# Performance work log

Measured on AMD Instinct MI355X. Metric: run time of the kernel, lower is better.

Reference implementation:

```python
import jax, jax.numpy as jnp
import numpy as np

N_EMBD = 384
N_HEAD = 6
HEAD_SIZE = N_EMBD // N_HEAD
D_FF = 4 * N_EMBD
LN_EPS = 1e-3  # keras LayerNormalization default epsilon


def setup_inputs() -> dict:
    key = jax.random.key(0)
    ks = jax.random.split(key, 12)
    B, T = 4, 2048
    s = 1.0 / np.sqrt(N_EMBD)
    return {
        "x": jax.random.normal(ks[0], (B, T, N_EMBD), dtype=jnp.float32),
        "Wq": jax.random.normal(ks[1], (N_EMBD, N_EMBD), dtype=jnp.float32) * s,
        "Wk": jax.random.normal(ks[2], (N_EMBD, N_EMBD), dtype=jnp.float32) * s,
        "Wv": jax.random.normal(ks[3], (N_EMBD, N_EMBD), dtype=jnp.float32) * s,
        "Wo": jax.random.normal(ks[4], (N_EMBD, N_EMBD), dtype=jnp.float32) * s,
        "bo": jnp.zeros((N_EMBD,), dtype=jnp.float32),
        "W1": jax.random.normal(ks[5], (N_EMBD, D_FF), dtype=jnp.float32) * s,
        "b1": jnp.zeros((D_FF,), dtype=jnp.float32),
        "W2": jax.random.normal(ks[6], (D_FF, N_EMBD), dtype=jnp.float32) * (1.0 / np.sqrt(D_FF)),
        "b2": jnp.zeros((N_EMBD,), dtype=jnp.float32),
        "g1": jnp.ones((N_EMBD,), dtype=jnp.float32),
        "be1": jnp.zeros((N_EMBD,), dtype=jnp.float32),
        "g2": jnp.ones((N_EMBD,), dtype=jnp.float32),
        "be2": jnp.zeros((N_EMBD,), dtype=jnp.float32),
    }


def _layer_norm(x, gamma, beta):
    mu = jnp.mean(x, axis=-1, keepdims=True)
    var = jnp.mean(jnp.square(x - mu), axis=-1, keepdims=True)
    return (x - mu) * jax.lax.rsqrt(var + LN_EPS) * gamma + beta


def _block(x, Wq, Wk, Wv, Wo, bo, W1, b1, W2, b2, g1, be1, g2, be2):
    B, T, C = x.shape
    H, D = N_HEAD, HEAD_SIZE
    q = (x @ Wq).reshape(B, T, H, D).transpose(0, 2, 1, 3)  # [B,H,T,D]
    k = (x @ Wk).reshape(B, T, H, D).transpose(0, 2, 1, 3)
    v = (x @ Wv).reshape(B, T, H, D).transpose(0, 2, 1, 3)
    scores = jnp.einsum("bhqd,bhkd->bhqk", q, k) / jnp.sqrt(jnp.float32(D))
    causal = jnp.tril(jnp.ones((T, T), dtype=bool))
    scores = jnp.where(causal, scores, jnp.float32(-1e9))
    attn = jax.nn.softmax(scores, axis=-1)  # dropout is identity at inference
    out = jnp.einsum("bhqk,bhkd->bhqd", attn, v)
    out = out.transpose(0, 2, 1, 3).reshape(B, T, H * D)
    y = out @ Wo + bo
    x = _layer_norm(x + y, g1, be1)
    y = jax.nn.relu(x @ W1 + b1) @ W2 + b2
    return _layer_norm(x + y, g2, be2)


def reference(x, Wq, Wk, Wv, Wo, bo, W1, b1, W2, b2, g1, be1, g2, be2):
    return _block(x, Wq, Wk, Wv, Wo, bo, W1, b1, W2, b2, g1, be1, g2, be2)
```

## Files before the change

### kernel.cpp

```cpp
#include <hip/hip_runtime.h>

#define C_DIM  384
#define HEADS  6
#define HD     64
#define FF_DIM 1536
#define LN_EPS 1e-3f
#define TSEQ   2048
#define BATCH  4
#define LOG2E  1.4426950408889634f
#define QK_SCALE 0.18033688011112042f

typedef __attribute__((ext_vector_type(4))) float          f32x4;
typedef __attribute__((ext_vector_type(4))) float          float4_t;
typedef __attribute__((ext_vector_type(8))) short          bfrag;
typedef __attribute__((ext_vector_type(4))) unsigned short ushort4_t;
typedef __attribute__((ext_vector_type(8))) unsigned short ushort8_t;

__device__ inline unsigned short f2bf(float f) {
    unsigned int u = __builtin_bit_cast(unsigned int, f);
    u += 0x7fff + ((u >> 16) & 1);
    return (unsigned short)(u >> 16);
}
__device__ inline unsigned short f2bf_t(float f) {
    return (unsigned short)(__builtin_bit_cast(unsigned int, f) >> 16);
}

__device__ inline void gload_lds16(const void* g, void* l) {
    __builtin_amdgcn_global_load_lds(
        (const __attribute__((address_space(1))) unsigned int*)g,
        (__attribute__((address_space(3))) unsigned int*)l,
        16, 0, 0);
}

__global__ __launch_bounds__(256)
void transpose_w4(const float* __restrict__ Wq, const float* __restrict__ Wk,
                  const float* __restrict__ Wv, const float* __restrict__ Wo,
                  unsigned short* __restrict__ Dq, unsigned short* __restrict__ Dk,
                  unsigned short* __restrict__ Dv, unsigned short* __restrict__ Do_)
{
    __shared__ float tile[32][33];
    const int z = blockIdx.z;
    const float* W = z == 0 ? Wq : (z == 1 ? Wk : (z == 2 ? Wv : Wo));
    unsigned short* D = z == 0 ? Dq : (z == 1 ? Dk : (z == 2 ? Dv : Do_));
    const int tx = threadIdx.x, ty = threadIdx.y;
    const int n0 = blockIdx.x * 32, k0 = blockIdx.y * 32;
    #pragma unroll
    for (int i = 0; i < 32; i += 8)
        tile[ty + i][tx] = W[(size_t)(k0 + ty + i) * C_DIM + n0 + tx];
    __syncthreads();
    #pragma unroll
    for (int i = 0; i < 32; i += 8)
        D[(size_t)(n0 + ty + i) * C_DIM + k0 + tx] = f2bf(tile[tx][ty + i]);
}

__global__ __launch_bounds__(256)
void transpose_w(const float* __restrict__ W, unsigned short* __restrict__ Wt, int K, int N)
{
    __shared__ float tile[32][33];
    const int tx = threadIdx.x, ty = threadIdx.y;
    const int n0 = blockIdx.x * 32, k0 = blockIdx.y * 32;
    #pragma unroll
    for (int i = 0; i < 32; i += 8)
        tile[ty + i][tx] = W[(size_t)(k0 + ty + i) * N + n0 + tx];
    __syncthreads();
    #pragma unroll
    for (int i = 0; i < 32; i += 8)
        Wt[(size_t)(n0 + ty + i) * K + k0 + tx] = f2bf(tile[tx][ty + i]);
}

__global__ __launch_bounds__(256)
void cvt_f32_bf16_x4(const float* __restrict__ in, unsigned short* __restrict__ out, int n4)
{
    int i = blockIdx.x * 256 + threadIdx.x;
    if (i >= n4) return;
    float4_t v = ((const float4_t*)in)[i];
    ushort4_t o = { f2bf(v.x), f2bf(v.y), f2bf(v.z), f2bf(v.w) };
    ((ushort4_t*)out)[i] = o;
}

__global__ __launch_bounds__(256)
void vtrans_kernel(const unsigned short* __restrict__ qkv,
                   unsigned short* __restrict__ vt,
                   unsigned short* __restrict__ ktc)
{
    __shared__ unsigned short tile[32][34];
    const int tx = threadIdx.x, ty = threadIdx.y;
    const int bh = blockIdx.z, b = bh / HEADS, h = bh % HEADS;
    const int t0 = blockIdx.x * 32, d0 = blockIdx.y * 32;
    #pragma unroll
    for (int i = 0; i < 32; i += 8) {
        tile[ty + i][tx] = qkv[(size_t)(b * TSEQ + t0 + ty + i) * 1152 + 2 * C_DIM + h * HD + d0 + tx];
        ktc[((size_t)bh * TSEQ + t0 + ty + i) * HD + d0 + tx] =
            qkv[(size_t)(b * TSEQ + t0 + ty + i) * 1152 + C_DIM + h * HD + d0 + tx];
    }
    __syncthreads();
    #pragma unroll
    for (int i = 0; i < 32; i += 8)
        vt[((size_t)bh * HD + d0 + ty + i) * TSEQ + t0 + tx] = tile[tx][ty + i];
}

template<int OBF16, int BIAS, int RELU, int QSCALE>
__global__ __launch_bounds__(256)
void gemm_lds(const unsigned short* __restrict__ A, const unsigned short* __restrict__ Bt,
              const float* __restrict__ bias, void* __restrict__ Cv,
              int M, int N, int K)
{
    __shared__ __align__(16) unsigned short As[16 * 512];
    __shared__ __align__(16) unsigned short Bs[16 * 512];

    const int t = threadIdx.x, lane = t & 63, w = t >> 6;
    const int ln16 = lane & 15, hi16 = lane >> 4;
    const int wr = w >> 1, wc = w & 1;
    const int row0 = blockIdx.y * 128, col0 = blockIdx.x * 128;

    f32x4 acc[4][4] = {};

    for (int k0 = 0; k0 < K; k0 += 64) {
        #pragma unroll
        for (int i = 0; i < 4; ++i) {
            const int f  = w * 4 + i;
            const int ks = f >> 3, rf = f & 7;
            const int row = rf * 16 + ln16;
            const int kc  = k0 + ks * 32 + hi16 * 8;
            gload_lds16(&A [(size_t)(row0 + row) * K + kc], &As[f * 512]);
            gload_lds16(&Bt[(size_t)(col0 + row) * K + kc], &Bs[f * 512]);
        }
        __syncthreads();
        #pragma unroll
        for (int ks = 0; ks < 2; ++ks) {
            bfrag a[4], b[4];
            #pragma unroll
            for (int i = 0; i < 4; ++i)
                a[i] = *(const bfrag*)&As[(ks * 8 + wr * 4 + i) * 512 + lane * 8];
            #pragma unroll
            for (int j = 0; j < 4; ++j)
                b[j] = *(const bfrag*)&Bs[(ks * 8 + wc * 4 + j) * 512 + lane * 8];
            #pragma unroll
            for (int i = 0; i < 4; ++i)
                #pragma unroll
                for (int j = 0; j < 4; ++j)
                    acc[i][j] = __builtin_amdgcn_mfma_f32_16x16x32_bf16(a[i], b[j], acc[i][j], 0, 0, 0);
        }
        __syncthreads();
    }

    #pragma unroll
    for (int j = 0; j < 4; ++j) {
        const int col = col0 + wc * 64 + j * 16 + ln16;
        const float bv = BIAS ? bias[col] : 0.0f;
        const float sc = (QSCALE && col < C_DIM) ? QK_SCALE : 1.0f;
        #pragma unroll
        for (int i = 0; i < 4; ++i) {
            #pragma unroll
            for (int e = 0; e < 4; ++e) {
                const int row = row0 + wr * 64 + i * 16 + hi16 * 4 + e;
                float v = acc[i][j][e] + bv;
                if (RELU) v = fmaxf(v, 0.0f);
                if (QSCALE) v *= sc;
                if (OBF16) ((unsigned short*)Cv)[(size_t)row * N + col] = f2bf(v);
                else       ((float*)Cv)[(size_t)row * N + col] = v;
            }
        }
    }
}

__device__ inline void qk16(const bfrag (&qf)[2][2], const bfrag (&kf)[4][2],
                            f32x4 (&sf)[2][4])
{
    #pragma unroll
    for (int jt = 0; jt < 4; ++jt)
        #pragma unroll
        for (int ks = 0; ks < 2; ++ks) {
            sf[0][jt] = __builtin_amdgcn_mfma_f32_16x16x32_bf16(qf[0][ks], kf[jt][ks], sf[0][jt], 0, 0, 0);
            sf[1][jt] = __builtin_amdgcn_mfma_f32_16x16x32_bf16(qf[1][ks], kf[jt][ks], sf[1][jt], 0, 0, 0);
        }
}

__device__ inline void softmax_pv(f32x4 (&sf)[2][4], const bfrag (&vf)[4][2],
                                  f32x4 (&acc)[2][4],
                                  float (&mrow)[2][4], float (&lrow)[2][4],
                                  unsigned short (*Ps)[72],
                                  int tok0, int kt, bool last, int ln16, int hi16)
{
    float lmax[2][4];
    bool need = false;
    #pragma unroll
    for (int rf = 0; rf < 2; ++rf)
        #pragma unroll
        for (int e = 0; e < 4; ++e) {
            const int row = tok0 + rf * 16 + hi16 * 4 + e;
            float mx = -1e30f;
            #pragma unroll
            for (int jt = 0; jt < 4; ++jt) {
                float sv = sf[rf][jt][e];
                if (last && (kt * 64 + jt * 16 + ln16 > row)) sv = -1e30f;
                mx = fmaxf(mx, sv);
            }
            lmax[rf][e] = mx;
            need = need || (mx > mrow[rf][e] + 8.0f);
        }
    if (__any(need)) {
        #pragma unroll
        for (int rf = 0; rf < 2; ++rf)
            #pragma unroll
            for (int e = 0; e < 4; ++e) {
                float rm = lmax[rf][e];
                rm = fmaxf(rm, __shfl_xor(rm, 1));
                rm = fmaxf(rm, __shfl_xor(rm, 2));
                rm = fmaxf(rm, __shfl_xor(rm, 4));
                rm = fmaxf(rm, __shfl_xor(rm, 8));
                const float mn = fmaxf(mrow[rf][e], rm);
                const float corr = exp2f(mrow[rf][e] - mn);
                mrow[rf][e] = mn;
                lrow[rf][e] *= corr;
                #pragma unroll
                for (int dt = 0; dt < 4; ++dt) acc[rf][dt][e] *= corr;
            }
    }

    #pragma unroll
    for (int rf = 0; rf < 2; ++rf)
        #pragma unroll
        for (int jt = 0; jt < 4; ++jt)
            #pragma unroll
            for (int e = 0; e < 4; ++e) {
                const int row = tok0 + rf * 16 + hi16 * 4 + e;
                float sv = sf[rf][jt][e];
                if (last && (kt * 64 + jt * 16 + ln16 > row)) sv = -1e30f;
                const float pe = exp2f(sv - mrow[rf][e]);
                lrow[rf][e] += pe;
                Ps[rf * 16 + hi16 * 4 + e][jt * 16 + ln16] = f2bf_t(pe);
            }

    bfrag pf[2][2];
    #pragma unroll
    for (int rf = 0; rf < 2; ++rf)
        #pragma unroll
        for (int ks = 0; ks < 2; ++ks)
            pf[rf][ks] = *(const bfrag*)&Ps[rf * 16 + ln16][ks * 32 + hi16 * 8];
    #pragma unroll
    for (int ks = 0; ks < 2; ++ks)
        #pragma unroll
        for (int rf = 0; rf < 2; ++rf)
            #pragma unroll
            for (int dt = 0; dt < 4; ++dt)
                acc[rf][dt] = __builtin_amdgcn_mfma_f32_16x16x32_bf16(pf[rf][ks], vf[dt][ks], acc[rf][dt], 0, 0, 0);
}

__global__ __launch_bounds__(64)
void attn_kernel(const unsigned short* __restrict__ qkv,
                 const unsigned short* __restrict__ ktc,
                 const unsigned short* __restrict__ vt,
                 unsigned short* __restrict__ att)
{
    __shared__ __align__(16) unsigned short Ps[32][72];
    const int lane = threadIdx.x;
    const int ln16 = lane & 15, hi16 = lane >> 4;
    const int bid = blockIdx.x;
    const int xcd = bid & 7;
    const int i2  = bid >> 3;
    const int bh  = xcd * 3 + (i2 >> 6);
    const int qw  = 63 - (i2 & 63);
    const int b   = bh / HEADS, h = bh % HEADS;
    const int tok0 = qw * 32;
    const size_t qrow0 = (size_t)b * TSEQ;
    const int NT = (qw >> 1) + 1;

    bfrag qf[2][2];
    #pragma unroll
    for (int rf = 0; rf < 2; ++rf)
        #pragma unroll
        for (int ks = 0; ks < 2; ++ks)
            qf[rf][ks] = *(const bfrag*)&qkv[(qrow0 + tok0 + rf * 16 + ln16) * 1152 + h * HD + ks * 32 + hi16 * 8];

    f32x4 acc[2][4] = {};
    float mrow[2][4], lrow[2][4];
    #pragma unroll
    for (int rf = 0; rf < 2; ++rf)
        #pragma unroll
        for (int e = 0; e < 4; ++e) { mrow[rf][e] = -1e30f; lrow[rf][e] = 0.0f; }

    const unsigned short* Kb = ktc + (size_t)bh * TSEQ * HD;
    const unsigned short* Vb = vt  + (size_t)bh * HD * TSEQ;

    auto loadK = [&](bfrag (&kf)[4][2], int kt) {
        #pragma unroll
        for (int jt = 0; jt < 4; ++jt)
            #pragma unroll
            for (int ks = 0; ks < 2; ++ks)
                kf[jt][ks] = *(const bfrag*)&Kb[(size_t)(kt * 64 + jt * 16 + ln16) * HD + ks * 32 + hi16 * 8];
    };
    auto loadV = [&](bfrag (&vf)[4][2], int kt) {
        #pragma unroll
        for (int dt = 0; dt < 4; ++dt)
            #pragma unroll
            for (int ks = 0; ks < 2; ++ks)
                vf[dt][ks] = *(const bfrag*)&Vb[(size_t)(dt * 16 + ln16) * TSEQ + kt * 64 + ks * 32 + hi16 * 8];
    };

    bfrag kfa[4][2], vfa[4][2], kfb[4][2], vfb[4][2];
    loadK(kfa, 0); loadV(vfa, 0);
    int kt = 0;
    for (;;) {
        if (kt + 1 < NT) { loadK(kfb, kt + 1); loadV(vfb, kt + 1); }
        {
            f32x4 sf[2][4] = {};
            qk16(qf, kfa, sf);
            softmax_pv(sf, vfa, acc, mrow, lrow, Ps, tok0, kt, kt == NT - 1, ln16, hi16);
        }
        if (++kt >= NT) break;
        if (kt + 1 < NT) { loadK(kfa, kt + 1); loadV(vfa, kt + 1); }
        {
            f32x4 sf[2][4] = {};
            qk16(qf, kfb, sf);
            softmax_pv(sf, vfb, acc, mrow, lrow, Ps, tok0, kt, kt == NT - 1, ln16, hi16);
        }
        if (++kt >= NT) break;
    }

    #pragma unroll
    for (int rf = 0; rf < 2; ++rf)
        #pragma unroll
        for (int e = 0; e < 4; ++e) {
            float l = lrow[rf][e];
            l += __shfl_xor(l, 1);
            l += __shfl_xor(l, 2);
            l += __shfl_xor(l, 4);
            l += __shfl_xor(l, 8);
            const float inv = 1.0f / l;
            const size_t row = qrow0 + tok0 + rf * 16 + hi16 * 4 + e;
            #pragma unroll
            for (int dt = 0; dt < 4; ++dt)
                att[row * C_DIM + h * HD + dt * 16 + ln16] = f2bf(acc[rf][dt][e] * inv);
        }
}

template<int WB>
__global__ __launch_bounds__(256)
void ln_residual_kernel(const float* __restrict__ A, const float* __restrict__ R,
                        const float* __restrict__ gamma, const float* __restrict__ beta,
                        float* __restrict__ out, unsigned short* __restrict__ outb, int Mrows)
{
    const int lane = threadIdx.x & 63;
    const int wv   = threadIdx.x >> 6;
    const int row  = blockIdx.x * 4 + wv;
    if (row >= Mrows) return;
    const size_t off = (size_t)row * C_DIM;

    float v[6];
    float sum = 0.0f;
    #pragma unroll
    for (int j = 0; j < 6; ++j) {
        const int c = lane + 64 * j;
        v[j] = A[off + c] + R[off + c];
        sum += v[j];
    }
    #pragma unroll
    for (int o = 1; o < 64; o <<= 1) sum += __shfl_xor(sum, o);
    const float mu = sum * (1.0f / C_DIM);

    float sq = 0.0f;
    #pragma unroll
    for (int j = 0; j < 6; ++j) { const float d = v[j] - mu; sq = fmaf(d, d, sq); }
    #pragma unroll
    for (int o = 1; o < 64; o <<= 1) sq += __shfl_xor(sq, o);
    const float rstd = rsqrtf(sq * (1.0f / C_DIM) + LN_EPS);

    #pragma unroll
    for (int j = 0; j < 6; ++j) {
        const int c = lane + 64 * j;
        const float r = (v[j] - mu) * rstd * gamma[c] + beta[c];
        out[off + c] = r;
        if (WB) outb[off + c] = f2bf(r);
    }
}

extern "C" void kernel_launch(void* const* d_in, const int* in_sizes, int n_in,
                              void* d_out, int out_size, void* d_ws, size_t ws_size,
                              hipStream_t stream)
{
    const float* x   = (const float*)d_in[0];
    const float* Wq  = (const float*)d_in[1];
    const float* Wk  = (const float*)d_in[2];
    const float* Wv  = (const float*)d_in[3];
    const float* Wo  = (const float*)d_in[4];
    const float* bo  = (const float*)d_in[5];
    const float* W1  = (const float*)d_in[6];
    const float* b1  = (const float*)d_in[7];
    const float* W2  = (const float*)d_in[8];
    const float* b2  = (const float*)d_in[9];
    const float* g1  = (const float*)d_in[10];
    const float* be1 = (const float*)d_in[11];
    const float* g2  = (const float*)d_in[12];
    const float* be2 = (const float*)d_in[13];
    float* out = (float*)d_out;

    const int M = BATCH * TSEQ;
    const size_t MC = (size_t)M * C_DIM;

    char* ws = (char*)d_ws;
    unsigned short* qkv = (unsigned short*)ws;
    unsigned short* vt  = (unsigned short*)(ws + (size_t)M*1152*2);
    unsigned short* att = (unsigned short*)(ws + (size_t)M*1152*2 + (size_t)BATCH*HEADS*HD*TSEQ*2);
    unsigned short* h1  = (unsigned short*)ws;
    char* p2 = ws + (size_t)M*1152*2 + (size_t)BATCH*HEADS*HD*TSEQ*2 + MC*2;
    unsigned short* xb  = (unsigned short*)p2;
    unsigned short* ktc = xb;
    float* y   = (float*)(p2 + MC*2);
    float* x1  = (float*)(p2 + MC*2 + MC*4);
    unsigned short* x1b = (unsigned short*)(p2 + MC*2 + 2*MC*4);
    char* p3 = p2 + MC*2 + 2*MC*4 + MC*2;
    unsigned short* Wqkv_t = (unsigned short*)p3;
    unsigned short* Wo_t   = Wqkv_t + (size_t)3*C_DIM*C_DIM;
    unsigned short* W1_t   = Wo_t   + (size_t)C_DIM*C_DIM;
    unsigned short* W2_t   = W1_t   + (size_t)FF_DIM*C_DIM;

    dim3 b256(256), b328(32, 8);

    transpose_w4<<<dim3(C_DIM/32, C_DIM/32, 4), b328, 0, stream>>>(
        Wq, Wk, Wv, Wo,
        Wqkv_t, Wqkv_t + (size_t)C_DIM*C_DIM, Wqkv_t + (size_t)2*C_DIM*C_DIM, Wo_t);
    transpose_w<<<dim3(FF_DIM/32, C_DIM/32), b328, 0, stream>>>(W1, W1_t, C_DIM, FF_DIM);
    transpose_w<<<dim3(C_DIM/32, FF_DIM/32), b328, 0, stream>>>(W2, W2_t, FF_DIM, C_DIM);

    cvt_f32_bf16_x4<<<dim3((MC/4 + 255)/256), b256, 0, stream>>>(x, xb, (int)(MC/4));

    gemm_lds<1, 0, 0, 1><<<dim3(3*C_DIM/128, M/128), b256, 0, stream>>>(
        xb, Wqkv_t, nullptr, qkv, M, 3*C_DIM, C_DIM);

    vtrans_kernel<<<dim3(TSEQ/32, HD/32, BATCH*HEADS), b328, 0, stream>>>(qkv, vt, ktc);

    attn_kernel<<<dim3(1536), dim3(64), 0, stream>>>(qkv, ktc, vt, att);

    gemm_lds<0, 1, 0, 0><<<dim3(C_DIM/128, M/128), b256, 0, stream>>>(
        att, Wo_t, bo, y, M, C_DIM, C_DIM);

    ln_residual_kernel<1><<<dim3(M/4), b256, 0, stream>>>(x, y, g1, be1, x1, x1b, M);

    gemm_lds<1, 1, 1, 0><<<dim3(FF_DIM/128, M/128), b256, 0, stream>>>(
        x1b, W1_t, b1, h1, M, FF_DIM, C_DIM);

    gemm_lds<0, 1, 0, 0><<<dim3(C_DIM/128, M/128), b256, 0, stream>>>(
        h1, W2_t, b2, y, M, C_DIM, FF_DIM);

    ln_residual_kernel<0><<<dim3(M/4), b256, 0, stream>>>(x1, y, g2, be2, out, nullptr, M);
}
```

Before: 223.3 us.

## Share K/V tiles across two query waves via double-buffered LDS staging

```diff
diff --git a/kernel.cpp b/kernel.cpp
--- a/kernel.cpp
+++ b/kernel.cpp
@@ -247,24 +247,29 @@
                 acc[rf][dt] = __builtin_amdgcn_mfma_f32_16x16x32_bf16(pf[rf][ks], vf[dt][ks], acc[rf][dt], 0, 0, 0);
 }
 
-__global__ __launch_bounds__(64)
+__global__ __launch_bounds__(128)
 void attn_kernel(const unsigned short* __restrict__ qkv,
                  const unsigned short* __restrict__ ktc,
                  const unsigned short* __restrict__ vt,
                  unsigned short* __restrict__ att)
 {
-    __shared__ __align__(16) unsigned short Ps[32][72];
-    const int lane = threadIdx.x;
+    __shared__ __align__(16) unsigned short Klds[2][4096];
+    __shared__ __align__(16) unsigned short Vlds[2][4096];
+    __shared__ __align__(16) unsigned short Ps[2][32][72];
+
+    const int tid  = threadIdx.x;
+    const int lane = tid & 63, wid = tid >> 6;
     const int ln16 = lane & 15, hi16 = lane >> 4;
     const int bid = blockIdx.x;
     const int xcd = bid & 7;
     const int i2  = bid >> 3;
-    const int bh  = xcd * 3 + (i2 >> 6);
-    const int qw  = 63 - (i2 & 63);
+    const int j   = i2 / 3;
+    const int bh  = xcd * 3 + (i2 % 3);
+    const int qw  = 63 - (j * 2 + wid);
     const int b   = bh / HEADS, h = bh % HEADS;
     const int tok0 = qw * 32;
     const size_t qrow0 = (size_t)b * TSEQ;
-    const int NT = (qw >> 1) + 1;
+    const int NT = 32 - j;
 
     bfrag qf[2][2];
     #pragma unroll
@@ -283,39 +288,51 @@
     const unsigned short* Kb = ktc + (size_t)bh * TSEQ * HD;
     const unsigned short* Vb = vt  + (size_t)bh * HD * TSEQ;
 
-    auto loadK = [&](bfrag (&kf)[4][2], int kt) {
+    int off[4][2];
+    #pragma unroll
+    for (int jt = 0; jt < 4; ++jt)
+        #pragma unroll
+        for (int ks = 0; ks < 2; ++ks) {
+            const int row = jt * 16 + ln16;
+            off[jt][ks] = row * 128 + ((ks * 64 + hi16 * 16) ^ ((row & 7) << 4));
+        }
+
+    auto stage = [&](int bf, int kt) {
+        #pragma unroll
+        for (int i = 0; i < 4; ++i) {
+            const int g   = wid * 4 + i;
+            const int c16 = g * 64 + lane;
+            const int r   = c16 >> 3;
+            const int s16 = (c16 & 7) ^ (r & 7);
+            gload_lds16(&Kb[(size_t)(kt * 64 + r) * HD + s16 * 8], &Klds[bf][g * 512]);
+            gload_lds16(&Vb[(size_t)r * TSEQ + kt * 64 + s16 * 8], &Vlds[bf][g * 512]);
+        }
+    };
+
+    int buf = 0;
+    stage(0, 0);
+    __syncthreads();
+
+    for (int kt = 0; kt < NT; ++kt) {
+        if (kt + 1 < NT) stage(buf ^ 1, kt + 1);
+
+        const char* Kb8 = (const char*)&Klds[buf][0];
+        const char* Vb8 = (const char*)&Vlds[buf][0];
+        bfrag kf[4][2], vf[4][2];
         #pragma unroll
         for (int jt = 0; jt < 4; ++jt)
             #pragma unroll
-            for (int ks = 0; ks < 2; ++ks)
-                kf[jt][ks] = *(const bfrag*)&Kb[(size_t)(kt * 64 + jt * 16 + ln16) * HD + ks * 32 + hi16 * 8];
-    };
-    auto loadV = [&](bfrag (&vf)[4][2], int kt) {
-        #pragma unroll
-        for (int dt = 0; dt < 4; ++dt)
-            #pragma unroll
-            for (int ks = 0; ks < 2; ++ks)
-                vf[dt][ks] = *(const bfrag*)&Vb[(size_t)(dt * 16 + ln16) * TSEQ + kt * 64 + ks * 32 + hi16 * 8];
-    };
-
-    bfrag kfa[4][2], vfa[4][2], kfb[4][2], vfb[4][2];
-    loadK(kfa, 0); loadV(vfa, 0);
-    int kt = 0;
-    for (;;) {
-        if (kt + 1 < NT) { loadK(kfb, kt + 1); loadV(vfb, kt + 1); }
-        {
-            f32x4 sf[2][4] = {};
-            qk16(qf, kfa, sf);
-            softmax_pv(sf, vfa, acc, mrow, lrow, Ps, tok0, kt, kt == NT - 1, ln16, hi16);
-        }
-        if (++kt >= NT) break;
-        if (kt + 1 < NT) { loadK(kfa, kt + 1); loadV(vfa, kt + 1); }
-        {
-            f32x4 sf[2][4] = {};
-            qk16(qf, kfb, sf);
-            softmax_pv(sf, vfb, acc, mrow, lrow, Ps, tok0, kt, kt == NT - 1, ln16, hi16);
-        }
-        if (++kt >= NT) break;
+            for (int ks = 0; ks < 2; ++ks) {
+                kf[jt][ks] = *(const bfrag*)(Kb8 + off[jt][ks]);
+                vf[jt][ks] = *(const bfrag*)(Vb8 + off[jt][ks]);
+            }
+
+        f32x4 sf[2][4] = {};
+        qk16(qf, kf, sf);
+        softmax_pv(sf, vf, acc, mrow, lrow, Ps[wid], tok0, kt, kt == NT - 1, ln16, hi16);
+
+        __syncthreads();
+        buf ^= 1;
     }
 
     #pragma unroll
@@ -430,7 +447,7 @@
 
     vtrans_kernel<<<dim3(TSEQ/32, HD/32, BATCH*HEADS), b328, 0, stream>>>(qkv, vt, ktc);
 
-    attn_kernel<<<dim3(1536), dim3(64), 0, stream>>>(qkv, ktc, vt, att);
+    attn_kernel<<<dim3(768), dim3(128), 0, stream>>>(qkv, ktc, vt, att);
 
     gemm_lds<0, 1, 0, 0><<<dim3(C_DIM/128, M/128), b256, 0, stream>>>(
         att, Wo_t, bo, y, M, C_DIM, C_DIM);
```

Measured after the change: 222.6 us. About the same (-0.3%).
